# Optimization experiments

Hardware: AMD Instinct MI355X
Metric: run time of the kernel (lower is better)

## Reference

```python
import jax, jax.numpy as jnp
import numpy as np

NEG_SLOPE = 0.01  # torch leaky_relu default

N_NODES = 100000
N_EDGES = 1600000
D = 64
N_BBOX = 4096


def setup_inputs() -> dict:
    key = jax.random.key(0)
    ks = jax.random.split(key, 9)
    x = jax.random.normal(ks[0], (N_NODES, D), dtype=jnp.float32)
    edge_index = jax.random.randint(ks[1], (2, N_EDGES), 0, N_NODES, dtype=jnp.int64)
    bbox = jax.random.randint(ks[2], (N_BBOX,), 0, N_NODES, dtype=jnp.int64)
    s = 1.0 / np.sqrt(D)
    W1_rel = jax.random.normal(ks[3], (D, D), dtype=jnp.float32) * s
    b1 = jax.random.normal(ks[4], (D,), dtype=jnp.float32) * s
    W1_root = jax.random.normal(ks[5], (D, D), dtype=jnp.float32) * s
    W2_rel = jax.random.normal(ks[6], (D, D), dtype=jnp.float32) * s
    b2 = jax.random.normal(ks[7], (D,), dtype=jnp.float32) * s
    W2_root = jax.random.normal(ks[8], (D, D), dtype=jnp.float32) * s
    return {"x": x, "edge_index": edge_index, "bbox": bbox,
            "W1_rel": W1_rel, "b1": b1, "W1_root": W1_root,
            "W2_rel": W2_rel, "b2": b2, "W2_root": W2_root}


def graph_conv(x, src, dst, W_rel, b, W_root):
    # PyG GraphConv: out_i = W_rel @ (sum_{j in N(i)} x_j) + b + W_root @ x_i
    msg = x[src]                                        # [E, D] gather
    agg = jax.ops.segment_sum(msg, dst, num_segments=x.shape[0])  # [N, D] scatter-add
    return agg @ W_rel + b + x @ W_root


def reference(x, edge_index, bbox, W1_rel, b1, W1_root, W2_rel, b2, W2_root):
    src, dst = edge_index[0], edge_index[1]
    h = graph_conv(x, src, dst, W1_rel, b1, W1_root)
    h = jax.nn.leaky_relu(h, NEG_SLOPE)
    # dropout is identity at inference (training=False)
    h = graph_conv(h, src, dst, W2_rel, b2, W2_root)
    h = jax.nn.leaky_relu(h, NEG_SLOPE)
    return h[bbox]
```

## Files before the change

### kernel.cpp

```cpp
#include <hip/hip_runtime.h>

#define N_NODES 100000
#define N_EDGES 1600000
#define D 64
#define N_BBOX 4096
#define CAP 64
#define NBITW 3136
#define NE4 (N_EDGES / 4)
#define NTILE1 (N_NODES / 16)
#define NTILE2 (N_BBOX / 16)

typedef short bf16x8 __attribute__((ext_vector_type(8)));
typedef float f32x4 __attribute__((ext_vector_type(4)));
typedef float f32x2 __attribute__((ext_vector_type(2)));

__device__ __forceinline__ int bperm(int srclane, int v) {
  return __builtin_amdgcn_ds_bpermute(srclane << 2, v);
}
__device__ __forceinline__ float lrelu(float v) {
  return fmaxf(v, 0.01f * v);
}
__device__ __forceinline__ bool testbit(const unsigned* bits, int i) {
  return (bits[i >> 5] >> (i & 31)) & 1u;
}
__device__ __forceinline__ short f2bf(float f) {
  unsigned u = __float_as_uint(f);
  u += 0x7FFFu + ((u >> 16) & 1u);
  return (short)(u >> 16);
}

__global__ __launch_bounds__(256) void zeromark_kernel(
    const int* __restrict__ bbox, unsigned* __restrict__ is_bbox_bits,
    unsigned* __restrict__ needed_bits) {
  const int t = threadIdx.x;
  for (int i = t; i < NBITW; i += 256) {
    is_bbox_bits[i] = 0u;
    needed_bits[i] = 0u;
  }
  __syncthreads();
  for (int i = t; i < N_BBOX; i += 256) {
    const int n = bbox[i];
    const unsigned m = 1u << (n & 31);
    atomicOr(&is_bbox_bits[n >> 5], m);
    atomicOr(&needed_bits[n >> 5], m);
  }
}

__global__ __launch_bounds__(256) void prep_kernel(const float4* __restrict__ x4,
                                                   bf16x8* __restrict__ xb,
                                                   uint2* __restrict__ xb8v,
                                                   const int* __restrict__ src,
                                                   const int4* __restrict__ dst4,
                                                   const unsigned* __restrict__ is_bbox_bits,
                                                   unsigned* __restrict__ needed_bits,
                                                   int* __restrict__ cnt,
                                                   const float* __restrict__ W1rel,
                                                   const float* __restrict__ W1root,
                                                   const float* __restrict__ W2rel,
                                                   const float* __restrict__ W2root,
                                                   short* __restrict__ wf) {
  const int i = blockIdx.x * 256 + threadIdx.x;
  if (i < N_NODES) cnt[i] = 0;
  if (i < N_NODES * 8) {
    const float4 a = x4[i * 2], b = x4[i * 2 + 1];
    bf16x8 r;
    r[0] = f2bf(a.x); r[1] = f2bf(a.y); r[2] = f2bf(a.z); r[3] = f2bf(a.w);
    r[4] = f2bf(b.x); r[5] = f2bf(b.y); r[6] = f2bf(b.z); r[7] = f2bf(b.w);
    xb[i] = r;
    int lo = __builtin_amdgcn_cvt_pk_fp8_f32(a.x, a.y, 0, false);
    lo = __builtin_amdgcn_cvt_pk_fp8_f32(a.z, a.w, lo, true);
    int hi = __builtin_amdgcn_cvt_pk_fp8_f32(b.x, b.y, 0, false);
    hi = __builtin_amdgcn_cvt_pk_fp8_f32(b.z, b.w, hi, true);
    uint2 w;
    w.x = (unsigned)lo;
    w.y = (unsigned)hi;
    xb8v[i] = w;
  } else {
    const int t = i - N_NODES * 8;
    if (t < 4 * 4096) {
      const int layer = t >> 13;
      const int r = t & 8191;
      const int m = r >> 12;
      const int e = r & 4095;
      const int kh = e >> 11, quad = (e >> 9) & 3;
      const int col = (e >> 3) & 63, ii = e & 7;
      const int k = kh * 32 + quad * 8 + ii;
      const float* W = layer ? (m ? W2root : W2rel) : (m ? W1root : W1rel);
      wf[t] = f2bf(W[k * 64 + col]);
    } else {
      const int e4 = t - 4 * 4096;
      if (e4 < NE4) {
        const int4 d = dst4[e4];
        const int eb = e4 * 4;
        if (testbit(is_bbox_bits, d.x))
          atomicOr(&needed_bits[src[eb] >> 5], 1u << (src[eb] & 31));
        if (testbit(is_bbox_bits, d.y))
          atomicOr(&needed_bits[src[eb + 1] >> 5], 1u << (src[eb + 1] & 31));
        if (testbit(is_bbox_bits, d.z))
          atomicOr(&needed_bits[src[eb + 2] >> 5], 1u << (src[eb + 2] & 31));
        if (testbit(is_bbox_bits, d.w))
          atomicOr(&needed_bits[src[eb + 3] >> 5], 1u << (src[eb + 3] & 31));
      }
    }
  }
}

__global__ __launch_bounds__(256) void scatter_kernel(
    const int4* __restrict__ src4, const int4* __restrict__ dst4,
    const unsigned* __restrict__ needed_bits, int* __restrict__ cnt,
    int* __restrict__ slots) {
  const int i4 = blockIdx.x * 256 + threadIdx.x;
  if (i4 >= NE4) return;
  const int4 d = dst4[i4];
  const int4 s = src4[i4];
#define SCAT(dd, ss)                                            \
  if (testbit(needed_bits, dd)) {                               \
    const int pos = atomicAdd(&cnt[dd], 1);                     \
    if (pos < CAP) slots[(size_t)(dd)*CAP + pos] = ss;          \
  }
  SCAT(d.x, s.x)
  SCAT(d.y, s.y)
  SCAT(d.z, s.z)
  SCAT(d.w, s.w)
#undef SCAT
}

__device__ __forceinline__ void gather_rows8(const uint2* __restrict__ rows,
                                             const int* __restrict__ slots,
                                             int node, int n, int lane,
                                             float accf[8]) {
  const int g = lane >> 3, c = lane & 7;
  const int myslot = (lane < n) ? slots[(size_t)node * CAP + lane] : 0;
#pragma unroll
  for (int i = 0; i < 8; i++) accf[i] = 0.f;
  for (int e0 = 0; e0 < n; e0 += 32) {
    const int rem = n - e0;
    int idx[4], s[4];
    uint2 v[4];
#pragma unroll
    for (int u = 0; u < 4; u++)
      if (u * 8 < rem) {
        idx[u] = e0 + u * 8 + g;
        s[u] = bperm(idx[u], myslot);
      }
#pragma unroll
    for (int u = 0; u < 4; u++)
      if (u * 8 < rem) {
        v[u] = make_uint2(0u, 0u);
        if (idx[u] < n) v[u] = rows[(size_t)s[u] * 8 + c];
      }
#pragma unroll
    for (int u = 0; u < 4; u++)
      if (u * 8 < rem) {
        f32x2 p;
        p = __builtin_amdgcn_cvt_pk_f32_fp8(v[u].x, false);
        accf[0] += p.x; accf[1] += p.y;
        p = __builtin_amdgcn_cvt_pk_f32_fp8(v[u].x, true);
        accf[2] += p.x; accf[3] += p.y;
        p = __builtin_amdgcn_cvt_pk_f32_fp8(v[u].y, false);
        accf[4] += p.x; accf[5] += p.y;
        p = __builtin_amdgcn_cvt_pk_f32_fp8(v[u].y, true);
        accf[6] += p.x; accf[7] += p.y;
      }
  }
#pragma unroll
  for (int off = 8; off < 64; off <<= 1)
#pragma unroll
    for (int i = 0; i < 8; i++) accf[i] += __shfl_xor(accf[i], off);
}

__device__ __forceinline__ void gather_rows(const uint4* __restrict__ rows,
                                            const int* __restrict__ slots,
                                            int node, int n, int lane,
                                            float accf[8]) {
  const int g = lane >> 3, c = lane & 7;
  const int myslot = (lane < n) ? slots[(size_t)node * CAP + lane] : 0;
#pragma unroll
  for (int i = 0; i < 8; i++) accf[i] = 0.f;
  for (int e0 = 0; e0 < n; e0 += 32) {
    const int rem = n - e0;
    int idx[4], s[4];
    uint4 v[4];
#pragma unroll
    for (int u = 0; u < 4; u++)
      if (u * 8 < rem) {
        idx[u] = e0 + u * 8 + g;
        s[u] = bperm(idx[u], myslot);
      }
#pragma unroll
    for (int u = 0; u < 4; u++)
      if (u * 8 < rem) {
        v[u] = make_uint4(0u, 0u, 0u, 0u);
        if (idx[u] < n) v[u] = rows[(size_t)s[u] * 8 + c];
      }
#pragma unroll
    for (int u = 0; u < 4; u++)
      if (u * 8 < rem) {
        accf[0] += __uint_as_float(v[u].x << 16);
        accf[1] += __uint_as_float(v[u].x & 0xFFFF0000u);
        accf[2] += __uint_as_float(v[u].y << 16);
        accf[3] += __uint_as_float(v[u].y & 0xFFFF0000u);
        accf[4] += __uint_as_float(v[u].z << 16);
        accf[5] += __uint_as_float(v[u].z & 0xFFFF0000u);
        accf[6] += __uint_as_float(v[u].w << 16);
        accf[7] += __uint_as_float(v[u].w & 0xFFFF0000u);
      }
  }
#pragma unroll
  for (int off = 8; off < 64; off <<= 1)
#pragma unroll
    for (int i = 0; i < 8; i++) accf[i] += __shfl_xor(accf[i], off);
}

__global__ __launch_bounds__(256) void gd1_kernel(
    const uint2* __restrict__ xb8v, const short* __restrict__ xb,
    const unsigned* __restrict__ needed_bits, const int* __restrict__ cnt,
    const int* __restrict__ slots, const short* __restrict__ wf1,
    const float* __restrict__ b1, short* __restrict__ hb) {
  __shared__ __align__(16) short aggt[16][72];
  const int t = threadIdx.x;
  const int lane = t & 63;
  const int wid = t >> 6;
  const int cn = lane & 15, quad = lane >> 4;
  const int col = wid * 16 + cn;
  const int node0 = blockIdx.x * 16;

  const bf16x8* wfv = (const bf16x8*)wf1;
  bf16x8 brel[2], broot[2];
#pragma unroll
  for (int kh = 0; kh < 2; kh++) {
    brel[kh] = wfv[(kh * 4 + quad) * 64 + col];
    broot[kh] = wfv[((2 + kh) * 4 + quad) * 64 + col];
  }
  const float bj = b1[col];

#pragma unroll
  for (int r4 = 0; r4 < 4; r4++) {
    const int row = wid * 4 + r4;
    const int node = node0 + row;
    int n = cnt[node];
    n = (n > CAP) ? CAP : n;
    if (n == 0) {
      if (lane < 8) {
        bf16x8 z = {0, 0, 0, 0, 0, 0, 0, 0};
        *(bf16x8*)(&aggt[row][lane * 8]) = z;
      }
      continue;
    }
    float accf[8];
    gather_rows8(xb8v, slots, node, n, lane, accf);
    if (lane < 8) {
      bf16x8 r;
#pragma unroll
      for (int i = 0; i < 8; i++) r[i] = f2bf(accf[i]);
      *(bf16x8*)(&aggt[row][lane * 8]) = r;
    }
  }
  __syncthreads();

  const int mrow = node0 + cn;
  const bool ndrow = testbit(needed_bits, mrow);
  f32x4 acc = {};
#pragma unroll
  for (int kh = 0; kh < 2; kh++) {
    const bf16x8 a_agg = *(const bf16x8*)(&aggt[cn][kh * 32 + quad * 8]);
    bf16x8 a_x = {0, 0, 0, 0, 0, 0, 0, 0};
    if (ndrow)
      a_x = *(const bf16x8*)(xb + (size_t)mrow * D + kh * 32 + quad * 8);
    acc = __builtin_amdgcn_mfma_f32_16x16x32_bf16(a_agg, brel[kh], acc, 0, 0, 0);
    acc = __builtin_amdgcn_mfma_f32_16x16x32_bf16(a_x, broot[kh], acc, 0, 0, 0);
  }
#pragma unroll
  for (int r = 0; r < 4; r++) {
    const int row = quad * 4 + r;
    if (testbit(needed_bits, node0 + row))
      hb[(size_t)(node0 + row) * D + col] = f2bf(lrelu(acc[r] + bj));
  }
}

__global__ __launch_bounds__(256) void gd2_kernel(
    const uint4* __restrict__ hb4, const short* __restrict__ hb,
    const int* __restrict__ cnt, const int* __restrict__ slots,
    const int* __restrict__ bbox, const short* __restrict__ wf2,
    const float* __restrict__ b2, float* __restrict__ out) {
  __shared__ __align__(16) short aggt[16][72];
  __shared__ int nodes_s[16];
  const int t = threadIdx.x;
  const int lane = t & 63;
  const int wid = t >> 6;
  const int cn = lane & 15, quad = lane >> 4;
  const int col = wid * 16 + cn;
  const int t0 = blockIdx.x * 16;

  if (t < 16) nodes_s[t] = bbox[t0 + t];

  const bf16x8* wfv = (const bf16x8*)wf2;
  bf16x8 brel[2], broot[2];
#pragma unroll
  for (int kh = 0; kh < 2; kh++) {
    brel[kh] = wfv[(kh * 4 + quad) * 64 + col];
    broot[kh] = wfv[((2 + kh) * 4 + quad) * 64 + col];
  }
  const float bj = b2[col];
  __syncthreads();

#pragma unroll
  for (int r4 = 0; r4 < 4; r4++) {
    const int row = wid * 4 + r4;
    const int node = nodes_s[row];
    int n = cnt[node];
    n = (n > CAP) ? CAP : n;
    if (n == 0) {
      if (lane < 8) {
        bf16x8 z = {0, 0, 0, 0, 0, 0, 0, 0};
        *(bf16x8*)(&aggt[row][lane * 8]) = z;
      }
      continue;
    }
    float accf[8];
    gather_rows(hb4, slots, node, n, lane, accf);
    if (lane < 8) {
      bf16x8 r;
#pragma unroll
      for (int i = 0; i < 8; i++) r[i] = f2bf(accf[i]);
      *(bf16x8*)(&aggt[row][lane * 8]) = r;
    }
  }
  __syncthreads();

  const int rnode = nodes_s[cn];
  f32x4 acc = {};
#pragma unroll
  for (int kh = 0; kh < 2; kh++) {
    const bf16x8 a_agg = *(const bf16x8*)(&aggt[cn][kh * 32 + quad * 8]);
    const bf16x8 a_h = *(const bf16x8*)(hb + (size_t)rnode * D + kh * 32 + quad * 8);
    acc = __builtin_amdgcn_mfma_f32_16x16x32_bf16(a_agg, brel[kh], acc, 0, 0, 0);
    acc = __builtin_amdgcn_mfma_f32_16x16x32_bf16(a_h, broot[kh], acc, 0, 0, 0);
  }
#pragma unroll
  for (int r = 0; r < 4; r++) {
    const int row = quad * 4 + r;
    out[(size_t)(t0 + row) * D + col] = lrelu(acc[r] + bj);
  }
}


extern "C" void kernel_launch(void* const* d_in, const int* in_sizes, int n_in,
                              void* d_out, int out_size, void* d_ws, size_t ws_size,
                              hipStream_t stream) {
  const float* x = (const float*)d_in[0];
  const int* ei = (const int*)d_in[1];
  const int* src = ei;
  const int* dst = ei + N_EDGES;
  const int* bbox = (const int*)d_in[2];
  const float* W1rel = (const float*)d_in[3];
  const float* b1 = (const float*)d_in[4];
  const float* W1root = (const float*)d_in[5];
  const float* W2rel = (const float*)d_in[6];
  const float* b2 = (const float*)d_in[7];
  const float* W2root = (const float*)d_in[8];
  float* out = (float*)d_out;

  char* ws = (char*)d_ws;
  size_t off = 0;
  auto alloc = [&](size_t bytes) -> char* {
    char* p = ws + off;
    off = (off + bytes + 511) & ~(size_t)511;
    return p;
  };
  unsigned* is_bbox_bits = (unsigned*)alloc(NBITW * sizeof(unsigned));
  unsigned* needed_bits = (unsigned*)alloc(NBITW * sizeof(unsigned));
  int* cnt = (int*)alloc(N_NODES * sizeof(int));
  int* slots = (int*)alloc((size_t)N_NODES * CAP * sizeof(int));
  short* xb = (short*)alloc((size_t)N_NODES * D * sizeof(short));
  unsigned char* xb8 = (unsigned char*)alloc((size_t)N_NODES * D);
  short* hb = (short*)alloc((size_t)N_NODES * D * sizeof(short));
  short* wf = (short*)alloc((size_t)4 * 4096 * sizeof(short));

  zeromark_kernel<<<1, 256, 0, stream>>>(bbox, is_bbox_bits, needed_bits);
  prep_kernel<<<(N_NODES * 8 + 4 * 4096 + NE4 + 255) / 256, 256, 0, stream>>>(
      (const float4*)x, (bf16x8*)xb, (uint2*)xb8, src, (const int4*)dst,
      is_bbox_bits, needed_bits, cnt, W1rel, W1root, W2rel, W2root, wf);
  scatter_kernel<<<(NE4 + 255) / 256, 256, 0, stream>>>(
      (const int4*)src, (const int4*)dst, needed_bits, cnt, slots);
  gd1_kernel<<<NTILE1, 256, 0, stream>>>((const uint2*)xb8, xb, needed_bits, cnt,
                                         slots, wf, b1, hb);
  gd2_kernel<<<NTILE2, 256, 0, stream>>>((const uint4*)hb, hb, cnt, slots, bbox,
                                         wf + 8192, b2, out);
}
```

Before: 195.8 us.

## Move x/weight conversion from prep into scatter kernel to overlap with edge scatter

The edge-marking pass now runs alone in a small kernel, and the fp32-to-bf16/fp8 conversion of x and the weight repacking move into the same launch as the slot scatter, split by block index. The aim is to shorten the critical path by overlapping the bandwidth-heavy conversion with the atomic-heavy scatter, instead of running conversion before the scatter dependency. Block counts are hardcoded, and the last conversion blocks index weights with t up to 4*4096 without an explicit bound check, which relies on NBLK_CV being exact.

Result: slower. 200.1 us (+2.2%).

```diff
diff --git a/kernel.cpp b/kernel.cpp
--- a/kernel.cpp
+++ b/kernel.cpp
@@ -7,6 +7,8 @@
 #define CAP 64
 #define NBITW 3136
 #define NE4 (N_EDGES / 4)
+#define NBLK_SC 1563
+#define NBLK_CV 3189
 #define NTILE1 (N_NODES / 16)
 #define NTILE2 (N_BBOX / 16)
 
@@ -46,38 +48,67 @@
   }
 }
 
-__global__ __launch_bounds__(256) void prep_kernel(const float4* __restrict__ x4,
-                                                   bf16x8* __restrict__ xb,
-                                                   uint2* __restrict__ xb8v,
-                                                   const int* __restrict__ src,
-                                                   const int4* __restrict__ dst4,
-                                                   const unsigned* __restrict__ is_bbox_bits,
-                                                   unsigned* __restrict__ needed_bits,
-                                                   int* __restrict__ cnt,
-                                                   const float* __restrict__ W1rel,
-                                                   const float* __restrict__ W1root,
-                                                   const float* __restrict__ W2rel,
-                                                   const float* __restrict__ W2root,
-                                                   short* __restrict__ wf) {
+__global__ __launch_bounds__(256) void markE_kernel(
+    const int* __restrict__ src, const int4* __restrict__ dst4,
+    const unsigned* __restrict__ is_bbox_bits,
+    unsigned* __restrict__ needed_bits, int* __restrict__ cnt) {
   const int i = blockIdx.x * 256 + threadIdx.x;
   if (i < N_NODES) cnt[i] = 0;
-  if (i < N_NODES * 8) {
-    const float4 a = x4[i * 2], b = x4[i * 2 + 1];
-    bf16x8 r;
-    r[0] = f2bf(a.x); r[1] = f2bf(a.y); r[2] = f2bf(a.z); r[3] = f2bf(a.w);
-    r[4] = f2bf(b.x); r[5] = f2bf(b.y); r[6] = f2bf(b.z); r[7] = f2bf(b.w);
-    xb[i] = r;
-    int lo = __builtin_amdgcn_cvt_pk_fp8_f32(a.x, a.y, 0, false);
-    lo = __builtin_amdgcn_cvt_pk_fp8_f32(a.z, a.w, lo, true);
-    int hi = __builtin_amdgcn_cvt_pk_fp8_f32(b.x, b.y, 0, false);
-    hi = __builtin_amdgcn_cvt_pk_fp8_f32(b.z, b.w, hi, true);
-    uint2 w;
-    w.x = (unsigned)lo;
-    w.y = (unsigned)hi;
-    xb8v[i] = w;
+  if (i < NE4) {
+    const int4 d = dst4[i];
+    const int eb = i * 4;
+    if (testbit(is_bbox_bits, d.x))
+      atomicOr(&needed_bits[src[eb] >> 5], 1u << (src[eb] & 31));
+    if (testbit(is_bbox_bits, d.y))
+      atomicOr(&needed_bits[src[eb + 1] >> 5], 1u << (src[eb + 1] & 31));
+    if (testbit(is_bbox_bits, d.z))
+      atomicOr(&needed_bits[src[eb + 2] >> 5], 1u << (src[eb + 2] & 31));
+    if (testbit(is_bbox_bits, d.w))
+      atomicOr(&needed_bits[src[eb + 3] >> 5], 1u << (src[eb + 3] & 31));
+  }
+}
+
+__global__ __launch_bounds__(256) void scatterX_kernel(
+    const int4* __restrict__ src4, const int4* __restrict__ dst4,
+    const unsigned* __restrict__ needed_bits, int* __restrict__ cnt,
+    int* __restrict__ slots, const float4* __restrict__ x4,
+    bf16x8* __restrict__ xb, uint2* __restrict__ xb8v,
+    const float* __restrict__ W1rel, const float* __restrict__ W1root,
+    const float* __restrict__ W2rel, const float* __restrict__ W2root,
+    short* __restrict__ wf) {
+  if (blockIdx.x < NBLK_SC) {
+    const int i4 = blockIdx.x * 256 + threadIdx.x;
+    if (i4 >= NE4) return;
+    const int4 d = dst4[i4];
+    const int4 s = src4[i4];
+#define SCAT(dd, ss)                                            \
+    if (testbit(needed_bits, dd)) {                             \
+      const int pos = atomicAdd(&cnt[dd], 1);                   \
+      if (pos < CAP) slots[(size_t)(dd)*CAP + pos] = ss;        \
+    }
+    SCAT(d.x, s.x)
+    SCAT(d.y, s.y)
+    SCAT(d.z, s.z)
+    SCAT(d.w, s.w)
+#undef SCAT
   } else {
-    const int t = i - N_NODES * 8;
-    if (t < 4 * 4096) {
+    const int i = (blockIdx.x - NBLK_SC) * 256 + threadIdx.x;
+    if (i < N_NODES * 8) {
+      const float4 a = x4[i * 2], b = x4[i * 2 + 1];
+      bf16x8 r;
+      r[0] = f2bf(a.x); r[1] = f2bf(a.y); r[2] = f2bf(a.z); r[3] = f2bf(a.w);
+      r[4] = f2bf(b.x); r[5] = f2bf(b.y); r[6] = f2bf(b.z); r[7] = f2bf(b.w);
+      xb[i] = r;
+      int lo = __builtin_amdgcn_cvt_pk_fp8_f32(a.x, a.y, 0, false);
+      lo = __builtin_amdgcn_cvt_pk_fp8_f32(a.z, a.w, lo, true);
+      int hi = __builtin_amdgcn_cvt_pk_fp8_f32(b.x, b.y, 0, false);
+      hi = __builtin_amdgcn_cvt_pk_fp8_f32(b.z, b.w, hi, true);
+      uint2 w;
+      w.x = (unsigned)lo;
+      w.y = (unsigned)hi;
+      xb8v[i] = w;
+    } else {
+      const int t = i - N_NODES * 8;
       const int layer = t >> 13;
       const int r = t & 8191;
       const int m = r >> 12;
@@ -87,42 +118,8 @@
       const int k = kh * 32 + quad * 8 + ii;
       const float* W = layer ? (m ? W2root : W2rel) : (m ? W1root : W1rel);
       wf[t] = f2bf(W[k * 64 + col]);
-    } else {
-      const int e4 = t - 4 * 4096;
-      if (e4 < NE4) {
-        const int4 d = dst4[e4];
-        const int eb = e4 * 4;
-        if (testbit(is_bbox_bits, d.x))
-          atomicOr(&needed_bits[src[eb] >> 5], 1u << (src[eb] & 31));
-        if (testbit(is_bbox_bits, d.y))
-          atomicOr(&needed_bits[src[eb + 1] >> 5], 1u << (src[eb + 1] & 31));
-        if (testbit(is_bbox_bits, d.z))
-          atomicOr(&needed_bits[src[eb + 2] >> 5], 1u << (src[eb + 2] & 31));
-        if (testbit(is_bbox_bits, d.w))
-          atomicOr(&needed_bits[src[eb + 3] >> 5], 1u << (src[eb + 3] & 31));
-      }
-    }
-  }
-}
-
-__global__ __launch_bounds__(256) void scatter_kernel(
-    const int4* __restrict__ src4, const int4* __restrict__ dst4,
-    const unsigned* __restrict__ needed_bits, int* __restrict__ cnt,
-    int* __restrict__ slots) {
-  const int i4 = blockIdx.x * 256 + threadIdx.x;
-  if (i4 >= NE4) return;
-  const int4 d = dst4[i4];
-  const int4 s = src4[i4];
-#define SCAT(dd, ss)                                            \
-  if (testbit(needed_bits, dd)) {                               \
-    const int pos = atomicAdd(&cnt[dd], 1);                     \
-    if (pos < CAP) slots[(size_t)(dd)*CAP + pos] = ss;          \
-  }
-  SCAT(d.x, s.x)
-  SCAT(d.y, s.y)
-  SCAT(d.z, s.z)
-  SCAT(d.w, s.w)
-#undef SCAT
+    }
+  }
 }
 
 __device__ __forceinline__ void gather_rows8(const uint2* __restrict__ rows,
@@ -378,11 +375,12 @@
   short* wf = (short*)alloc((size_t)4 * 4096 * sizeof(short));
 
   zeromark_kernel<<<1, 256, 0, stream>>>(bbox, is_bbox_bits, needed_bits);
-  prep_kernel<<<(N_NODES * 8 + 4 * 4096 + NE4 + 255) / 256, 256, 0, stream>>>(
-      (const float4*)x, (bf16x8*)xb, (uint2*)xb8, src, (const int4*)dst,
-      is_bbox_bits, needed_bits, cnt, W1rel, W1root, W2rel, W2root, wf);
-  scatter_kernel<<<(NE4 + 255) / 256, 256, 0, stream>>>(
-      (const int4*)src, (const int4*)dst, needed_bits, cnt, slots);
+  markE_kernel<<<NBLK_SC, 256, 0, stream>>>(src, (const int4*)dst,
+                                            is_bbox_bits, needed_bits, cnt);
+  scatterX_kernel<<<NBLK_SC + NBLK_CV, 256, 0, stream>>>(
+      (const int4*)src, (const int4*)dst, needed_bits, cnt, slots,
+      (const float4*)x, (bf16x8*)xb, (uint2*)xb8, W1rel, W1root, W2rel,
+      W2root, wf);
   gd1_kernel<<<NTILE1, 256, 0, stream>>>((const uint2*)xb8, xb, needed_bits, cnt,
                                          slots, wf, b1, hb);
   gd2_kernel<<<NTILE2, 256, 0, stream>>>((const uint4*)hb, hb, cnt, slots, bbox,
```
